# Performance work log

Measured on AMD Instinct MI355X. Metric: run time of the kernel, lower is better.

## Reference

```python
import jax, jax.numpy as jnp
import numpy as np

N_QUBITS = 4
N_LAYERS = 6
BATCH = 262144


def _apply_1q(state, U, wire):
    """Apply a 1-qubit gate U ((2,2) shared or (B,2,2) per-sample) on `wire`.
    state: (B, 2, 2, ..., 2) with n qubit axes after the batch axis."""
    s = jnp.moveaxis(state, 1 + wire, -1)
    shp = s.shape
    s2 = s.reshape(shp[0], -1, 2)
    if U.ndim == 3:
        s2 = jnp.einsum('bij,bkj->bki', U, s2)
    else:
        s2 = jnp.einsum('ij,bkj->bki', U, s2)
    return jnp.moveaxis(s2.reshape(shp), -1, 1 + wire)


def _apply_cnot(state, control, target):
    s = jnp.moveaxis(state, (1 + control, 1 + target), (-2, -1))
    shp = s.shape
    s2 = s.reshape(shp[0], -1, 2, 2)
    # flip target amplitudes where control bit is 1
    s2 = jnp.stack([s2[..., 0, :], s2[..., 1, ::-1]], axis=-2)
    return jnp.moveaxis(s2.reshape(shp), (-2, -1), (1 + control, 1 + target))


def _ry_batched(x):
    """RY(x) for x: (B,) -> (B,2,2) complex64 (real-valued matrix)."""
    c, s = jnp.cos(x / 2), jnp.sin(x / 2)
    m = jnp.stack([jnp.stack([c, -s], -1), jnp.stack([s, c], -1)], -2)
    return m.astype(jnp.complex64)


def _rot(phi, theta, omega):
    """qml.Rot = RZ(omega) RY(theta) RZ(phi), (2,2) complex64."""
    c, s = jnp.cos(theta / 2), jnp.sin(theta / 2)
    e = lambda a: jnp.exp(1j * a)
    m00 = e(-(phi + omega) / 2) * c
    m01 = -e((phi - omega) / 2) * s
    m10 = e(-(phi - omega) / 2) * s
    m11 = e((phi + omega) / 2) * c
    return jnp.stack([jnp.stack([m00, m01]), jnp.stack([m10, m11])]).astype(jnp.complex64)


def setup_inputs() -> dict:
    key = jax.random.key(0)
    k1, k2 = jax.random.split(key)
    inputs = jax.random.normal(k1, (BATCH, N_QUBITS), dtype=jnp.float32)
    quantum_weights = jax.random.uniform(k2, (N_LAYERS, N_QUBITS, 3), dtype=jnp.float32, minval=-0.05, maxval=0.05)
    return {"inputs": inputs, "quantum_weights": quantum_weights}


def reference(inputs, quantum_weights):
    B, n = inputs.shape
    L = quantum_weights.shape[0]
    # |0...0> state, batched
    state = jnp.zeros((B,) + (2,) * n, jnp.complex64)
    state = state.at[(slice(None),) + (0,) * n].set(1.0)
    # AngleEmbedding(rotation='Y'): RY(inputs[:, w]) on wire w
    for w in range(n):
        state = _apply_1q(state, _ry_batched(inputs[:, w]), w)
    # StronglyEntanglingLayers: Rot per wire, then ring of CNOTs with range r = l % (n-1) + 1
    for l in range(L):
        for w in range(n):
            state = _apply_1q(state, _rot(quantum_weights[l, w, 0], quantum_weights[l, w, 1], quantum_weights[l, w, 2]), w)
        r = l % (n - 1) + 1
        for w in range(n):
            state = _apply_cnot(state, w, (w + r) % n)
    # <Z_w> for each wire
    p = jnp.abs(state.reshape(B, -1)) ** 2  # (B, 2^n)
    bits = (jnp.arange(2 ** n)[:, None] >> jnp.arange(n - 1, -1, -1)[None, :]) & 1
    z = (1 - 2 * bits).astype(p.dtype)  # (2^n, n)
    return p @ z  # (B, n) float32
```

## Files before the change

### kernel.cpp

```cpp
#include <hip/hip_runtime.h>

#define N_QUBITS 4
#define N_LAYERS 6
#define NSTATES  16

__device__ __forceinline__ float2 cmul(float2 a, float2 b) {
    return make_float2(a.x * b.x - a.y * b.y, a.x * b.y + a.y * b.x);
}
__device__ __forceinline__ float2 cadd(float2 a, float2 b) {
    return make_float2(a.x + b.x, a.y + b.y);
}

__global__ __launch_bounds__(256) void build_u_kernel(
        const float* __restrict__ weights, float* __restrict__ U) {
    __shared__ float2 rotm[N_LAYERS * N_QUBITS][4];
    __shared__ float2 st[NSTATES][NSTATES];

    const int t = threadIdx.x;
    if (t < N_LAYERS * N_QUBITS) {
        const float phi   = weights[t * 3 + 0];
        const float theta = weights[t * 3 + 1];
        const float omega = weights[t * 3 + 2];
        float stheta, ctheta;
        sincosf(theta * 0.5f, &stheta, &ctheta);
        const float a1 = -(phi + omega) * 0.5f;
        const float a2 =  (phi - omega) * 0.5f;
        float s1, c1, s2, c2;
        sincosf(a1, &s1, &c1);
        sincosf(a2, &s2, &c2);
        rotm[t][0] = make_float2( c1 * ctheta,  s1 * ctheta);
        rotm[t][1] = make_float2(-c2 * stheta, -s2 * stheta);
        rotm[t][2] = make_float2( c2 * stheta, -s2 * stheta);
        rotm[t][3] = make_float2( c1 * ctheta, -s1 * ctheta);
    }

    const int c = t >> 4;
    const int i = t & 15;
    st[c][i] = make_float2(i == c ? 1.0f : 0.0f, 0.0f);
    __syncthreads();

    #pragma unroll 1
    for (int l = 0; l < N_LAYERS; ++l) {
        #pragma unroll 1
        for (int w = 0; w < N_QUBITS; ++w) {
            const int bit = 8 >> w;
            if (!(i & bit)) {
                const int j = i | bit;
                const float2 a0 = st[c][i];
                const float2 a1v = st[c][j];
                const float2 m00 = rotm[l * N_QUBITS + w][0];
                const float2 m01 = rotm[l * N_QUBITS + w][1];
                const float2 m10 = rotm[l * N_QUBITS + w][2];
                const float2 m11 = rotm[l * N_QUBITS + w][3];
                st[c][i] = cadd(cmul(m00, a0), cmul(m01, a1v));
                st[c][j] = cadd(cmul(m10, a0), cmul(m11, a1v));
            }
            __syncthreads();
        }
        const int r = l % (N_QUBITS - 1) + 1;
        int fi = i;
        #pragma unroll
        for (int w = 0; w < N_QUBITS; ++w) {
            const int tb = 8 >> ((w + r) & 3);
            if ((fi >> (3 - w)) & 1) fi ^= tb;
        }
        const float2 a = st[c][i];
        __syncthreads();
        st[c][fi] = a;
        __syncthreads();
    }

    U[2 * (i * NSTATES + c) + 0] = st[c][i].x;
    U[2 * (i * NSTATES + c) + 1] = st[c][i].y;
}

__global__ __launch_bounds__(256) void qc_apply_kernel(
        const float* __restrict__ inputs,
        const float* __restrict__ U,
        float* __restrict__ out,
        int B) {
    const int b = blockIdx.x * blockDim.x + threadIdx.x;
    if (b >= B) return;

    const float4 xin = reinterpret_cast<const float4*>(inputs)[b];
    float s0, c0, s1, c1, s2, c2, s3, c3;
    __sincosf(xin.x * 0.5f, &s0, &c0);
    __sincosf(xin.y * 0.5f, &s1, &c1);
    __sincosf(xin.z * 0.5f, &s2, &c2);
    __sincosf(xin.w * 0.5f, &s3, &c3);

    const float vA[4] = { c0 * c1, c0 * s1, s0 * c1, s0 * s1 };
    const float vB[4] = { c2 * c3, c2 * s3, s2 * c3, s2 * s3 };
    float v[NSTATES];
    #pragma unroll
    for (int a = 0; a < 4; ++a)
        #pragma unroll
        for (int q = 0; q < 4; ++q)
            v[a * 4 + q] = vA[a] * vB[q];

    float p[NSTATES];
    #pragma unroll
    for (int i = 0; i < NSTATES; ++i) {
        const float4* row = reinterpret_cast<const float4*>(U + 2 * NSTATES * i);
        float re = 0.0f, im = 0.0f;
        #pragma unroll
        for (int q = 0; q < 8; ++q) {
            const float4 u4 = row[q];
            re = fmaf(u4.x, v[2 * q],     re);
            im = fmaf(u4.y, v[2 * q],     im);
            re = fmaf(u4.z, v[2 * q + 1], re);
            im = fmaf(u4.w, v[2 * q + 1], im);
        }
        p[i] = re * re + im * im;
    }

    float sa[8], da[8];
    #pragma unroll
    for (int j = 0; j < 8; ++j) {
        sa[j] = p[2 * j] + p[2 * j + 1];
        da[j] = p[2 * j] - p[2 * j + 1];
    }
    const float z3 = ((da[0] + da[1]) + (da[2] + da[3])) +
                     ((da[4] + da[5]) + (da[6] + da[7]));
    float sb[4], db[4];
    #pragma unroll
    for (int j = 0; j < 4; ++j) {
        sb[j] = sa[2 * j] + sa[2 * j + 1];
        db[j] = sa[2 * j] - sa[2 * j + 1];
    }
    const float z2 = (db[0] + db[1]) + (db[2] + db[3]);
    const float z1 = (sb[0] - sb[1]) + (sb[2] - sb[3]);
    const float z0 = (sb[0] + sb[1]) - (sb[2] + sb[3]);

    reinterpret_cast<float4*>(out)[b] = make_float4(z0, z1, z2, z3);
}

extern "C" void kernel_launch(void* const* d_in, const int* in_sizes, int n_in,
                              void* d_out, int out_size, void* d_ws, size_t ws_size,
                              hipStream_t stream) {
    const float* inputs  = (const float*)d_in[0];
    const float* weights = (const float*)d_in[1];
    float* out = (float*)d_out;
    float* U   = (float*)d_ws;
    const int B = in_sizes[0] / N_QUBITS;

    build_u_kernel<<<1, 256, 0, stream>>>(weights, U);

    const int block = 256;
    const int grid = (B + block - 1) / block;
    qc_apply_kernel<<<grid, block, 0, stream>>>(inputs, U, out, B);
}
```

Baseline: 68.98 us.

## Fuse unitary construction into apply kernel, recomputing U per block in LDS

Merges the single-block unitary-building kernel into the batch kernel, so every block rebuilds the 16x16 circuit unitary in shared memory and then applies it to two samples per thread. This removes the second launch and the serial dependency on a one-block kernel, and reads U from LDS instead of global memory. The cost is that each of the 512 blocks redoes the 24-gate simulation, with about 30 barriers, before any useful work starts.

```diff
diff --git a/kernel.cpp b/kernel.cpp
--- a/kernel.cpp
+++ b/kernel.cpp
@@ -3,6 +3,7 @@
 #define N_QUBITS 4
 #define N_LAYERS 6
 #define NSTATES  16
+#define SPT      2
 
 __device__ __forceinline__ float2 cmul(float2 a, float2 b) {
     return make_float2(a.x * b.x - a.y * b.y, a.x * b.y + a.y * b.x);
@@ -11,27 +12,32 @@
     return make_float2(a.x + b.x, a.y + b.y);
 }
 
-__global__ __launch_bounds__(256) void build_u_kernel(
-        const float* __restrict__ weights, float* __restrict__ U) {
+__global__ __launch_bounds__(256) void qc_fused_kernel(
+        const float* __restrict__ inputs,
+        const float* __restrict__ weights,
+        float* __restrict__ out,
+        int B) {
     __shared__ float2 rotm[N_LAYERS * N_QUBITS][4];
     __shared__ float2 st[NSTATES][NSTATES];
+    __shared__ float  Ut[NSTATES][2 * NSTATES];
 
     const int t = threadIdx.x;
+
     if (t < N_LAYERS * N_QUBITS) {
         const float phi   = weights[t * 3 + 0];
         const float theta = weights[t * 3 + 1];
         const float omega = weights[t * 3 + 2];
-        float stheta, ctheta;
-        sincosf(theta * 0.5f, &stheta, &ctheta);
+        float sth, cth;
+        sincosf(theta * 0.5f, &sth, &cth);
         const float a1 = -(phi + omega) * 0.5f;
         const float a2 =  (phi - omega) * 0.5f;
         float s1, c1, s2, c2;
         sincosf(a1, &s1, &c1);
         sincosf(a2, &s2, &c2);
-        rotm[t][0] = make_float2( c1 * ctheta,  s1 * ctheta);
-        rotm[t][1] = make_float2(-c2 * stheta, -s2 * stheta);
-        rotm[t][2] = make_float2( c2 * stheta, -s2 * stheta);
-        rotm[t][3] = make_float2( c1 * ctheta, -s1 * ctheta);
+        rotm[t][0] = make_float2( c1 * cth,  s1 * cth);
+        rotm[t][1] = make_float2(-c2 * sth, -s2 * sth);
+        rotm[t][2] = make_float2( c2 * sth, -s2 * sth);
+        rotm[t][3] = make_float2( c1 * cth, -s1 * cth);
     }
 
     const int c = t >> 4;
@@ -70,69 +76,67 @@
         __syncthreads();
     }
 
-    U[2 * (i * NSTATES + c) + 0] = st[c][i].x;
-    U[2 * (i * NSTATES + c) + 1] = st[c][i].y;
-}
+    Ut[i][2 * c + 0] = st[c][i].x;
+    Ut[i][2 * c + 1] = st[c][i].y;
+    __syncthreads();
 
-__global__ __launch_bounds__(256) void qc_apply_kernel(
-        const float* __restrict__ inputs,
-        const float* __restrict__ U,
-        float* __restrict__ out,
-        int B) {
-    const int b = blockIdx.x * blockDim.x + threadIdx.x;
-    if (b >= B) return;
+    #pragma unroll
+    for (int sidx = 0; sidx < SPT; ++sidx) {
+        const int b = blockIdx.x * (blockDim.x * SPT) + sidx * blockDim.x + t;
+        if (b >= B) continue;
 
-    const float4 xin = reinterpret_cast<const float4*>(inputs)[b];
-    float s0, c0, s1, c1, s2, c2, s3, c3;
-    __sincosf(xin.x * 0.5f, &s0, &c0);
-    __sincosf(xin.y * 0.5f, &s1, &c1);
-    __sincosf(xin.z * 0.5f, &s2, &c2);
-    __sincosf(xin.w * 0.5f, &s3, &c3);
+        const float4 xin = reinterpret_cast<const float4*>(inputs)[b];
+        float s0, c0, s1, c1, s2, c2, s3, c3;
+        __sincosf(xin.x * 0.5f, &s0, &c0);
+        __sincosf(xin.y * 0.5f, &s1, &c1);
+        __sincosf(xin.z * 0.5f, &s2, &c2);
+        __sincosf(xin.w * 0.5f, &s3, &c3);
 
-    const float vA[4] = { c0 * c1, c0 * s1, s0 * c1, s0 * s1 };
-    const float vB[4] = { c2 * c3, c2 * s3, s2 * c3, s2 * s3 };
-    float v[NSTATES];
-    #pragma unroll
-    for (int a = 0; a < 4; ++a)
+        const float vA[4] = { c0 * c1, c0 * s1, s0 * c1, s0 * s1 };
+        const float vB[4] = { c2 * c3, c2 * s3, s2 * c3, s2 * s3 };
+        float v[NSTATES];
         #pragma unroll
-        for (int q = 0; q < 4; ++q)
-            v[a * 4 + q] = vA[a] * vB[q];
+        for (int a = 0; a < 4; ++a)
+            #pragma unroll
+            for (int q = 0; q < 4; ++q)
+                v[a * 4 + q] = vA[a] * vB[q];
 
-    float p[NSTATES];
-    #pragma unroll
-    for (int i = 0; i < NSTATES; ++i) {
-        const float4* row = reinterpret_cast<const float4*>(U + 2 * NSTATES * i);
-        float re = 0.0f, im = 0.0f;
+        float p[NSTATES];
         #pragma unroll
-        for (int q = 0; q < 8; ++q) {
-            const float4 u4 = row[q];
-            re = fmaf(u4.x, v[2 * q],     re);
-            im = fmaf(u4.y, v[2 * q],     im);
-            re = fmaf(u4.z, v[2 * q + 1], re);
-            im = fmaf(u4.w, v[2 * q + 1], im);
+        for (int row = 0; row < NSTATES; ++row) {
+            const float4* r4 = reinterpret_cast<const float4*>(&Ut[row][0]);
+            float re = 0.0f, im = 0.0f;
+            #pragma unroll
+            for (int q = 0; q < 8; ++q) {
+                const float4 u4 = r4[q];
+                re = fmaf(u4.x, v[2 * q],     re);
+                im = fmaf(u4.y, v[2 * q],     im);
+                re = fmaf(u4.z, v[2 * q + 1], re);
+                im = fmaf(u4.w, v[2 * q + 1], im);
+            }
+            p[row] = re * re + im * im;
         }
-        p[i] = re * re + im * im;
+
+        float sa[8], da[8];
+        #pragma unroll
+        for (int j = 0; j < 8; ++j) {
+            sa[j] = p[2 * j] + p[2 * j + 1];
+            da[j] = p[2 * j] - p[2 * j + 1];
+        }
+        const float z3 = ((da[0] + da[1]) + (da[2] + da[3])) +
+                         ((da[4] + da[5]) + (da[6] + da[7]));
+        float sb[4], db[4];
+        #pragma unroll
+        for (int j = 0; j < 4; ++j) {
+            sb[j] = sa[2 * j] + sa[2 * j + 1];
+            db[j] = sa[2 * j] - sa[2 * j + 1];
+        }
+        const float z2 = (db[0] + db[1]) + (db[2] + db[3]);
+        const float z1 = (sb[0] - sb[1]) + (sb[2] - sb[3]);
+        const float z0 = (sb[0] + sb[1]) - (sb[2] + sb[3]);
+
+        reinterpret_cast<float4*>(out)[b] = make_float4(z0, z1, z2, z3);
     }
-
-    float sa[8], da[8];
-    #pragma unroll
-    for (int j = 0; j < 8; ++j) {
-        sa[j] = p[2 * j] + p[2 * j + 1];
-        da[j] = p[2 * j] - p[2 * j + 1];
-    }
-    const float z3 = ((da[0] + da[1]) + (da[2] + da[3])) +
-                     ((da[4] + da[5]) + (da[6] + da[7]));
-    float sb[4], db[4];
-    #pragma unroll
-    for (int j = 0; j < 4; ++j) {
-        sb[j] = sa[2 * j] + sa[2 * j + 1];
-        db[j] = sa[2 * j] - sa[2 * j + 1];
-    }
-    const float z2 = (db[0] + db[1]) + (db[2] + db[3]);
-    const float z1 = (sb[0] - sb[1]) + (sb[2] - sb[3]);
-    const float z0 = (sb[0] + sb[1]) - (sb[2] + sb[3]);
-
-    reinterpret_cast<float4*>(out)[b] = make_float4(z0, z1, z2, z3);
 }
 
 extern "C" void kernel_launch(void* const* d_in, const int* in_sizes, int n_in,
@@ -141,12 +145,9 @@
     const float* inputs  = (const float*)d_in[0];
     const float* weights = (const float*)d_in[1];
     float* out = (float*)d_out;
-    float* U   = (float*)d_ws;
     const int B = in_sizes[0] / N_QUBITS;
 
-    build_u_kernel<<<1, 256, 0, stream>>>(weights, U);
-
     const int block = 256;
-    const int grid = (B + block - 1) / block;
-    qc_apply_kernel<<<grid, block, 0, stream>>>(inputs, U, out, B);
+    const int grid = (B + block * SPT - 1) / (block * SPT);
+    qc_fused_kernel<<<grid, block, 0, stream>>>(inputs, weights, out, B);
 }
```

After: 73.42 us. 6.4% more time.
